# Kernel tuning notes

Measured on AMD Instinct MI355X. Metric: run time of the kernel, lower is better.

The kernel has to match this reference:

```python
import jax, jax.numpy as jnp
import numpy as np

N = 100000
E = 1600000
IN_C, HID_C, OUT_C = 128, 128, 64
BN_EPS = 1e-5


def setup_inputs() -> dict:
    key = jax.random.key(0)
    ks = jax.random.split(key, 8)
    x = jax.random.normal(ks[0], (N, IN_C), dtype=jnp.float32)
    edge_index = jax.random.randint(ks[1], (2, E), 0, N, dtype=jnp.int64)
    # GCNConv: Linear(in, out, bias=False) + separate bias added after aggregation
    W1 = jax.random.normal(ks[2], (IN_C, HID_C), dtype=jnp.float32) / np.sqrt(IN_C)
    b1 = jnp.zeros((HID_C,), dtype=jnp.float32)
    gamma = jnp.ones((HID_C,), dtype=jnp.float32)
    beta = jnp.zeros((HID_C,), dtype=jnp.float32)
    W2 = jax.random.normal(ks[3], (HID_C, OUT_C), dtype=jnp.float32) / np.sqrt(HID_C)
    b2 = jnp.zeros((OUT_C,), dtype=jnp.float32)
    return {"x": x, "edge_index": edge_index, "W1": W1, "b1": b1,
            "gamma": gamma, "beta": beta, "W2": W2, "b2": b2}


def _gcn_norm(edge_index, n):
    # add self-loops, symmetric normalization deg^-1/2 * deg^-1/2 (PyG gcn_norm)
    loop = jnp.arange(n, dtype=edge_index.dtype)
    row = jnp.concatenate([edge_index[0], loop])  # source (j)
    col = jnp.concatenate([edge_index[1], loop])  # target (i)
    deg = jax.ops.segment_sum(jnp.ones_like(col, dtype=jnp.float32), col, num_segments=n)
    d_inv_sqrt = jnp.where(deg > 0, jax.lax.rsqrt(deg), 0.0)
    norm = d_inv_sqrt[row] * d_inv_sqrt[col]  # [E + N]
    return row, col, norm


def _gcn_conv(h, W, b, row, col, norm, n):
    h = h @ W                                        # [N, out]
    msg = h[row] * norm[:, None]                     # gather + scale  [E+N, out]
    agg = jax.ops.segment_sum(msg, col, num_segments=n)  # scatter-add [N, out]
    return agg + b


def _batchnorm(h, gamma, beta):
    mean = jnp.mean(h, axis=0)
    var = jnp.mean(jnp.square(h - mean), axis=0)
    return (h - mean) * jax.lax.rsqrt(var + BN_EPS) * gamma + beta


def reference(x, edge_index, W1, b1, gamma, beta, W2, b2):
    n = x.shape[0]
    row, col, norm = _gcn_norm(edge_index, n)
    h = _gcn_conv(x, W1, b1, row, col, norm, n)
    h = _batchnorm(h, gamma, beta)
    h = jax.nn.relu(h)
    # dropout is identity in deterministic/eval reference
    out = _gcn_conv(h, W2, b2, row, col, norm, n)
    return out
```

## Files before the change

### kernel.cpp

```cpp
#include <hip/hip_runtime.h>

#define IN_C 128
#define HID_C 128
#define OUT_C 64
#define BN_EPS 1e-5f
#define BUCK_SHIFT 6
#define MAXBUCK 2048
#define CHUNK_SHIFT 13

typedef unsigned short ushort_t;
typedef __attribute__((ext_vector_type(8))) short bf16x8;
typedef __attribute__((ext_vector_type(4))) float f32x4;
typedef __attribute__((ext_vector_type(8))) unsigned short u16x8;

__device__ __forceinline__ float bf2f(ushort_t u) {
  union { unsigned i; float f; } c; c.i = (unsigned)u << 16; return c.f;
}
__device__ __forceinline__ ushort_t f2bf(float f) {
  union { float f; unsigned u; } c; c.f = f;
  unsigned r = c.u + 0x7FFF + ((c.u >> 16) & 1);
  return (ushort_t)(r >> 16);
}


__global__ __launch_bounds__(256) void k_hist(const int* __restrict__ col,
                                              int* __restrict__ ghist,
                                              int e, int nbuck, int chunk) {
  __shared__ int h[MAXBUCK];
  for (int p = threadIdx.x; p < nbuck; p += 256) h[p] = 0;
  __syncthreads();
  int s = blockIdx.x * chunk;
  int t = min(s + chunk, e);
  for (int i = s + threadIdx.x; i < t; i += 256)
    atomicAdd(&h[col[i] >> BUCK_SHIFT], 1);
  __syncthreads();
  int* gh = ghist + (size_t)blockIdx.x * nbuck;
  for (int p = threadIdx.x; p < nbuck; p += 256) gh[p] = h[p];
}

__global__ __launch_bounds__(256) void k_s1(int* __restrict__ ghist,
                                            int* __restrict__ btotal, int nbuck) {
  __shared__ int sd[256];
  int p = blockIdx.x;
  int tid = threadIdx.x;
  int idx = tid * nbuck + p;
  int v = ghist[idx];
  sd[tid] = v;
  __syncthreads();
  for (int off = 1; off < 256; off <<= 1) {
    int t = (tid >= off) ? sd[tid - off] : 0;
    __syncthreads();
    sd[tid] += t;
    __syncthreads();
  }
  ghist[idx] = sd[tid] - v;
  if (tid == 255) btotal[p] = sd[255];
}

__global__ __launch_bounds__(512) void k_s2(const int* __restrict__ btotal,
                                            int* __restrict__ bstart,
                                            int nbuck, int e,
                                            int* __restrict__ rowptr, int n) {
  __shared__ int sd[512];
  int tid = threadIdx.x;
  int base = tid * 4;
  int v[4]; int s = 0;
#pragma unroll
  for (int q = 0; q < 4; q++) {
    int i = base + q;
    v[q] = (i < nbuck) ? btotal[i] : 0;
    s += v[q];
  }
  sd[tid] = s;
  __syncthreads();
  for (int off = 1; off < 512; off <<= 1) {
    int t = (tid >= off) ? sd[tid - off] : 0;
    __syncthreads();
    sd[tid] += t;
    __syncthreads();
  }
  int run = sd[tid] - s;
#pragma unroll
  for (int q = 0; q < 4; q++) {
    int i = base + q;
    if (i < nbuck) bstart[i] = run;
    run += v[q];
  }
  if (tid == 0) { bstart[nbuck] = e; rowptr[n] = e; }
}

__global__ __launch_bounds__(256) void k_scatter(const int* __restrict__ row,
                                                 const int* __restrict__ col,
                                                 const int* __restrict__ ghist,
                                                 const int* __restrict__ bstart,
                                                 unsigned* __restrict__ bpack,
                                                 int e, int nbuck, int chunk) {
  __shared__ int cur[MAXBUCK];
  const int* gh = ghist + (size_t)blockIdx.x * nbuck;
  for (int p = threadIdx.x; p < nbuck; p += 256) cur[p] = bstart[p] + gh[p];
  __syncthreads();
  int s = blockIdx.x * chunk;
  int t = min(s + chunk, e);
  for (int i = s + threadIdx.x; i < t; i += 256) {
    int c = col[i];
    int pos = atomicAdd(&cur[c >> BUCK_SHIFT], 1);
    bpack[pos] = ((unsigned)(c & 63) << 17) | (unsigned)row[i];
  }
}

__global__ __launch_bounds__(256) void k_bsort(const unsigned* __restrict__ bpack,
                                               const int* __restrict__ bstart,
                                               int* __restrict__ rowptr,
                                               float* __restrict__ dis,
                                               int* __restrict__ srcidx, int n) {
  __shared__ int cnt[1024];
  __shared__ int excl[1025];
  __shared__ int sd[256];
  __shared__ int sbs, sbe;
  int tid = threadIdx.x;
  int p = blockIdx.x;
  for (int q = tid; q < 1024; q += 256) cnt[q] = 0;
  if (tid == 0) { sbs = bstart[p]; sbe = bstart[p + 1]; }
  __syncthreads();
  int bs = sbs, be = sbe;
  for (int i = bs + tid; i < be; i += 256) {
    unsigned v = bpack[i];
    int key = (int)((v >> 17) << 4) | (int)((v & 0x1FFFFu) >> CHUNK_SHIFT);
    atomicAdd(&cnt[key], 1);
  }
  __syncthreads();
  int base = tid * 4;
  int c0 = cnt[base], c1 = cnt[base + 1], c2 = cnt[base + 2], c3 = cnt[base + 3];
  int s = c0 + c1 + c2 + c3;
  sd[tid] = s;
  __syncthreads();
  for (int off = 1; off < 256; off <<= 1) {
    int t = (tid >= off) ? sd[tid - off] : 0;
    __syncthreads();
    sd[tid] += t;
    __syncthreads();
  }
  int run = sd[tid] - s;
  excl[base] = run;
  excl[base + 1] = run + c0;
  excl[base + 2] = run + c0 + c1;
  excl[base + 3] = run + c0 + c1 + c2;
  if (tid == 255) excl[1024] = sd[255];
  __syncthreads();
  if (tid < 64) {
    int st = excl[tid * 16];
    int en = excl[(tid + 1) * 16];
    int node = (p << BUCK_SHIFT) + tid;
    if (node < n) {
      rowptr[node] = bs + st;
      dis[node] = rsqrtf((float)(en - st + 1));
    }
  }
  __syncthreads();
  for (int i = bs + tid; i < be; i += 256) {
    unsigned v = bpack[i];
    int key = (int)((v >> 17) << 4) | (int)((v & 0x1FFFFu) >> CHUNK_SHIFT);
    int q = atomicAdd(&excl[key], 1);
    srcidx[bs + q] = (int)(v & 0x1FFFFu);
  }
}


__global__ void k_wpack(const float* __restrict__ W1, const float* __restrict__ W2,
                        ushort_t* __restrict__ WB1, ushort_t* __restrict__ WB2,
                        float* __restrict__ stats) {
  int idx = blockIdx.x * 256 + threadIdx.x;
  if (blockIdx.x == 0) stats[threadIdx.x] = 0.f;
  if (idx < 128 * 128) {
    int nn = idx >> 7, k = idx & 127;
    WB1[idx] = f2bf(W1[k * HID_C + nn]);
  }
  int idx2 = idx - 128 * 128;
  if (idx2 >= 0 && idx2 < 64 * 128) {
    int nn = idx2 >> 7, k = idx2 & 127;
    WB2[idx2] = f2bf(W2[k * OUT_C + nn]);
  }
}


__global__ __launch_bounds__(256) void k_gemm1_mfma(const float* __restrict__ x,
                                                    const ushort_t* __restrict__ WB,
                                                    const float* __restrict__ dis,
                                                    ushort_t* __restrict__ h1, int n) {
  int wave = threadIdx.x >> 6;
  int lane = threadIdx.x & 63;
  int m = lane & 15;
  int kg = lane >> 4;
  int rowbase = blockIdx.x * 64 + wave * 16;
  int rrow = rowbase + m; if (rrow >= n) rrow = n - 1;
  const float* xrow = x + (size_t)rrow * IN_C + kg * 8;
  f32x4 acc[8] = {};
#pragma unroll
  for (int ks = 0; ks < 4; ks++) {
    float4 a0 = *reinterpret_cast<const float4*>(xrow + ks * 32);
    float4 a1 = *reinterpret_cast<const float4*>(xrow + ks * 32 + 4);
    bf16x8 a;
    a[0] = (short)f2bf(a0.x); a[1] = (short)f2bf(a0.y);
    a[2] = (short)f2bf(a0.z); a[3] = (short)f2bf(a0.w);
    a[4] = (short)f2bf(a1.x); a[5] = (short)f2bf(a1.y);
    a[6] = (short)f2bf(a1.z); a[7] = (short)f2bf(a1.w);
#pragma unroll
    for (int nt = 0; nt < 8; nt++) {
      bf16x8 b = *reinterpret_cast<const bf16x8*>(WB + (nt * 16 + m) * 128 + ks * 32 + kg * 8);
      acc[nt] = __builtin_amdgcn_mfma_f32_16x16x32_bf16(a, b, acc[nt], 0, 0, 0);
    }
  }
#pragma unroll
  for (int r = 0; r < 4; r++) {
    int rowi = rowbase + kg * 4 + r;
    if (rowi < n) {
      float dr = dis[rowi];
#pragma unroll
      for (int nt = 0; nt < 8; nt++)
        h1[(size_t)rowi * HID_C + nt * 16 + m] = f2bf(dr * acc[nt][r]);
    }
  }
}


__global__ __launch_bounds__(256) void k_gemm2_mfma(const ushort_t* __restrict__ aggb,
                                                    const ushort_t* __restrict__ WB,
                                                    const float* __restrict__ stats,
                                                    const float* __restrict__ gamma,
                                                    const float* __restrict__ beta,
                                                    const float* __restrict__ dis,
                                                    ushort_t* __restrict__ h2, int n) {
  __shared__ float bnp_s[256];
  int tid = threadIdx.x;
  if (tid < 128) {
    float inv_n = 1.f / (float)n;
    float mean = stats[tid] * inv_n;
    float var = stats[128 + tid] * inv_n - mean * mean;
    float istd = rsqrtf(var + BN_EPS);
    float sc = gamma[tid] * istd;
    bnp_s[tid] = sc;
    bnp_s[128 + tid] = beta[tid] - mean * sc;
  }
  __syncthreads();
  int wave = tid >> 6;
  int lane = tid & 63;
  int m = lane & 15;
  int kg = lane >> 4;
  int rowbase = blockIdx.x * 64 + wave * 16;
  int rrow = rowbase + m; if (rrow >= n) rrow = n - 1;
  const ushort_t* arow = aggb + (size_t)rrow * HID_C + kg * 8;
  f32x4 acc[4] = {};
#pragma unroll
  for (int ks = 0; ks < 4; ks++) {
    int kbase = ks * 32 + kg * 8;
    u16x8 av = *reinterpret_cast<const u16x8*>(arow + ks * 32);
    float v[8];
#pragma unroll
    for (int q = 0; q < 8; q++)
      v[q] = bf2f(av[q]) * bnp_s[kbase + q] + bnp_s[128 + kbase + q];
    bf16x8 a;
#pragma unroll
    for (int q = 0; q < 8; q++) a[q] = (short)f2bf(v[q] > 0.f ? v[q] : 0.f);
#pragma unroll
    for (int nt = 0; nt < 4; nt++) {
      bf16x8 b = *reinterpret_cast<const bf16x8*>(WB + (nt * 16 + m) * 128 + ks * 32 + kg * 8);
      acc[nt] = __builtin_amdgcn_mfma_f32_16x16x32_bf16(a, b, acc[nt], 0, 0, 0);
    }
  }
#pragma unroll
  for (int r = 0; r < 4; r++) {
    int rowi = rowbase + kg * 4 + r;
    if (rowi < n) {
      float dr = dis[rowi];
#pragma unroll
      for (int nt = 0; nt < 4; nt++)
        h2[(size_t)rowi * OUT_C + nt * 16 + m] = f2bf(dr * acc[nt][r]);
    }
  }
}


__global__ __launch_bounds__(256) void k_spmm1_bf(const ushort_t* __restrict__ h,
                                                  const float* __restrict__ dis,
                                                  const int* __restrict__ rowptr,
                                                  const int* __restrict__ srcidx,
                                                  const float* __restrict__ bias,
                                                  ushort_t* __restrict__ outp, int n) {
  constexpr int C = HID_C;
  constexpr int LPR = C / 8;
  constexpr int ROWS = 256 / LPR;
  int tid = threadIdx.x;
  int lane = tid & (LPR - 1);
  int r = tid / LPR;
  int i = blockIdx.x * ROWS + r;
  if (i >= n) return;
  int c8 = lane * 8;
  const ushort_t* hb = h + c8;

  float acc[8];
  u16x8 hv = *reinterpret_cast<const u16x8*>(hb + (size_t)i * C);
#pragma unroll
  for (int q = 0; q < 8; q++) acc[q] = bf2f(hv[q]);

  int s = rowptr[i], t = rowptr[i + 1];
  int p = s;
  for (; p + 16 <= t; p += 16) {
    int j[16]; u16x8 v[16];
#pragma unroll
    for (int k = 0; k < 16; k++) j[k] = srcidx[p + k];
#pragma unroll
    for (int k = 0; k < 16; k++)
      v[k] = *reinterpret_cast<const u16x8*>(hb + (size_t)j[k] * C);
#pragma unroll
    for (int k = 0; k < 16; k++)
#pragma unroll
      for (int q = 0; q < 8; q++) acc[q] += bf2f(v[k][q]);
  }
  for (; p + 4 <= t; p += 4) {
    int j[4]; u16x8 v[4];
#pragma unroll
    for (int k = 0; k < 4; k++) j[k] = srcidx[p + k];
#pragma unroll
    for (int k = 0; k < 4; k++)
      v[k] = *reinterpret_cast<const u16x8*>(hb + (size_t)j[k] * C);
#pragma unroll
    for (int k = 0; k < 4; k++)
#pragma unroll
      for (int q = 0; q < 8; q++) acc[q] += bf2f(v[k][q]);
  }
  for (; p < t; p++) {
    int j = srcidx[p];
    u16x8 v = *reinterpret_cast<const u16x8*>(hb + (size_t)j * C);
#pragma unroll
    for (int q = 0; q < 8; q++) acc[q] += bf2f(v[q]);
  }

  float di = dis[i];
  float4 b0 = *reinterpret_cast<const float4*>(bias + c8);
  float4 b1v = *reinterpret_cast<const float4*>(bias + c8 + 4);
  u16x8 o;
  o[0] = f2bf(di * acc[0] + b0.x);  o[1] = f2bf(di * acc[1] + b0.y);
  o[2] = f2bf(di * acc[2] + b0.z);  o[3] = f2bf(di * acc[3] + b0.w);
  o[4] = f2bf(di * acc[4] + b1v.x); o[5] = f2bf(di * acc[5] + b1v.y);
  o[6] = f2bf(di * acc[6] + b1v.z); o[7] = f2bf(di * acc[7] + b1v.w);
  *reinterpret_cast<u16x8*>(outp + (size_t)i * C + c8) = o;
}


__global__ __launch_bounds__(256) void k_spmm2_bf(const ushort_t* __restrict__ h,
                                                  const float* __restrict__ dis,
                                                  const int* __restrict__ rowptr,
                                                  const int* __restrict__ srcidx,
                                                  const float* __restrict__ bias,
                                                  float* __restrict__ outp, int n) {
  constexpr int C = OUT_C;
  constexpr int LPR = C / 8;
  constexpr int ROWS = 256 / LPR;
  int tid = threadIdx.x;
  int lane = tid & (LPR - 1);
  int r = tid / LPR;
  int i = blockIdx.x * ROWS + r;
  if (i >= n) return;
  int c8 = lane * 8;
  const ushort_t* hb = h + c8;

  float acc[8];
  u16x8 hv = *reinterpret_cast<const u16x8*>(hb + (size_t)i * C);
#pragma unroll
  for (int q = 0; q < 8; q++) acc[q] = bf2f(hv[q]);

  int s = rowptr[i], t = rowptr[i + 1];
  int p = s;
  for (; p + 16 <= t; p += 16) {
    int j[16]; u16x8 v[16];
#pragma unroll
    for (int k = 0; k < 16; k++) j[k] = srcidx[p + k];
#pragma unroll
    for (int k = 0; k < 16; k++)
      v[k] = *reinterpret_cast<const u16x8*>(hb + (size_t)j[k] * C);
#pragma unroll
    for (int k = 0; k < 16; k++)
#pragma unroll
      for (int q = 0; q < 8; q++) acc[q] += bf2f(v[k][q]);
  }
  for (; p + 4 <= t; p += 4) {
    int j[4]; u16x8 v[4];
#pragma unroll
    for (int k = 0; k < 4; k++) j[k] = srcidx[p + k];
#pragma unroll
    for (int k = 0; k < 4; k++)
      v[k] = *reinterpret_cast<const u16x8*>(hb + (size_t)j[k] * C);
#pragma unroll
    for (int k = 0; k < 4; k++)
#pragma unroll
      for (int q = 0; q < 8; q++) acc[q] += bf2f(v[k][q]);
  }
  for (; p < t; p++) {
    int j = srcidx[p];
    u16x8 v = *reinterpret_cast<const u16x8*>(hb + (size_t)j * C);
#pragma unroll
    for (int q = 0; q < 8; q++) acc[q] += bf2f(v[q]);
  }

  float di = dis[i];
  float4 b0 = *reinterpret_cast<const float4*>(bias + c8);
  float4 b1v = *reinterpret_cast<const float4*>(bias + c8 + 4);
  float4 o0, o1;
  o0.x = di * acc[0] + b0.x;  o0.y = di * acc[1] + b0.y;
  o0.z = di * acc[2] + b0.z;  o0.w = di * acc[3] + b0.w;
  o1.x = di * acc[4] + b1v.x; o1.y = di * acc[5] + b1v.y;
  o1.z = di * acc[6] + b1v.z; o1.w = di * acc[7] + b1v.w;
  float* op = outp + (size_t)i * C + c8;
  *reinterpret_cast<float4*>(op) = o0;
  *reinterpret_cast<float4*>(op + 4) = o1;
}


__global__ __launch_bounds__(256) void k_bnstats(const ushort_t* __restrict__ aggb,
                                                 float* __restrict__ stats, int n) {
  __shared__ float lsum[256 * 8];
  __shared__ float lsq[256 * 8];
  int tid = threadIdx.x;
  int lane = tid & 15;
  int rg = tid >> 4;
  float s[8] = {}, q[8] = {};
  for (int row = blockIdx.x * 16 + rg; row < n; row += gridDim.x * 16) {
    u16x8 v = *reinterpret_cast<const u16x8*>(aggb + (size_t)row * HID_C + lane * 8);
#pragma unroll
    for (int k = 0; k < 8; k++) {
      float f = bf2f(v[k]);
      s[k] += f;
      q[k] += f * f;
    }
  }
#pragma unroll
  for (int k = 0; k < 8; k++) { lsum[tid * 8 + k] = s[k]; lsq[tid * 8 + k] = q[k]; }
  __syncthreads();
  if (tid < 128) {
    int ln = tid >> 3, k = tid & 7;
    float ss = 0.f, qq = 0.f;
    for (int r = 0; r < 16; r++) {
      int idx = ((r << 4) + ln) * 8 + k;
      ss += lsum[idx];
      qq += lsq[idx];
    }
    atomicAdd(&stats[tid], ss);
    atomicAdd(&stats[128 + tid], qq);
  }
}


extern "C" void kernel_launch(void* const* d_in, const int* in_sizes, int n_in,
                              void* d_out, int out_size, void* d_ws, size_t ws_size,
                              hipStream_t stream) {
  const float* x     = (const float*)d_in[0];
  const int*   edge  = (const int*)d_in[1];
  const float* W1    = (const float*)d_in[2];
  const float* b1    = (const float*)d_in[3];
  const float* gamma = (const float*)d_in[4];
  const float* beta  = (const float*)d_in[5];
  const float* W2    = (const float*)d_in[6];
  const float* b2    = (const float*)d_in[7];
  float* out = (float*)d_out;

  int n = in_sizes[0] / IN_C;
  int e = in_sizes[1] / 2;
  int n64 = ((n + 63) / 64) * 64;
  int nbuck = (n + 63) >> BUCK_SHIFT;
  const int* row = edge;
  const int* col = edge + e;

  char* ws = (char*)d_ws;
  size_t off = 0;
  auto alloc = [&](size_t bytes) {
    void* p = ws + off;
    off = (off + bytes + 255) & ~(size_t)255;
    return p;
  };
  float*    dis   = (float*)alloc((size_t)n * 4);
  int*      rowp  = (int*)alloc((size_t)(n + 1) * 4);
  int*      srci  = (int*)alloc((size_t)e * 4);
  ushort_t* WB1   = (ushort_t*)alloc(128 * 128 * 2);
  ushort_t* WB2   = (ushort_t*)alloc(64 * 128 * 2);
  ushort_t* h1b   = (ushort_t*)alloc((size_t)n64 * HID_C * 2);
  ushort_t* aggb  = (ushort_t*)alloc((size_t)n64 * HID_C * 2);
  ushort_t* h2b   = (ushort_t*)alloc((size_t)n64 * OUT_C * 2);
  float*    stats = (float*)alloc(256 * 4);
  char* tr = (char*)aggb;
  unsigned* bpack = (unsigned*)tr;                       tr += (size_t)e * 4;
  int* ghist  = (int*)tr;                                tr += (size_t)256 * nbuck * 4;
  int* btotal = (int*)tr;                                tr += (size_t)(nbuck + 1) * 4;
  int* bstart = (int*)tr;
  (void)ws_size; (void)n_in; (void)out_size;

  int chunk = (e + 255) / 256;
  int nb64 = n64 / 64;

  k_wpack  <<<96, 256, 0, stream>>>(W1, W2, WB1, WB2, stats);
  k_hist   <<<256, 256, 0, stream>>>(col, ghist, e, nbuck, chunk);
  k_s1     <<<nbuck, 256, 0, stream>>>(ghist, btotal, nbuck);
  k_s2     <<<1, 512, 0, stream>>>(btotal, bstart, nbuck, e, rowp, n);
  k_scatter<<<256, 256, 0, stream>>>(row, col, ghist, bstart, bpack, e, nbuck, chunk);
  k_bsort  <<<nbuck, 256, 0, stream>>>(bpack, bstart, rowp, dis, srci, n);
  k_gemm1_mfma<<<nb64, 256, 0, stream>>>(x, WB1, dis, h1b, n);
  k_spmm1_bf<<<(n + 15) / 16, 256, 0, stream>>>(h1b, dis, rowp, srci, b1, aggb, n);
  k_bnstats<<<512, 256, 0, stream>>>(aggb, stats, n);
  k_gemm2_mfma<<<nb64, 256, 0, stream>>>(aggb, WB2, stats, gamma, beta, dis, h2b, n);
  k_spmm2_bf<<<(n + 31) / 32, 256, 0, stream>>>(h2b, dis, rowp, srci, b2, out, n);
}
```

Measured before the change: 231.0 us.

## Use 64 histogram chunks with bucket-major ghist and wave-shuffle prefix scan

Cuts the number of edge chunks in the bucket histogram/scatter from 256 to 64 and stores the per-chunk histogram bucket-major, so each bucket's chunk counts are contiguous. The per-bucket exclusive scan becomes a single 64-lane wave shuffle scan, with four buckets per block, replacing a 256-thread LDS scan full of barriers. The aim is to shrink the histogram buffer and the cost of the scan kernel. In exchange, the histogram and scatter kernels launch only 64 blocks, which may leave much of the GPU idle during those passes.

Result: slower. 282.0 us (+22.1%).

```diff
diff --git a/kernel.cpp b/kernel.cpp
--- a/kernel.cpp
+++ b/kernel.cpp
@@ -7,6 +7,7 @@
 #define BUCK_SHIFT 6
 #define MAXBUCK 2048
 #define CHUNK_SHIFT 13
+#define NSB 64
 
 typedef unsigned short ushort_t;
 typedef __attribute__((ext_vector_type(8))) short bf16x8;
@@ -34,27 +35,26 @@
   for (int i = s + threadIdx.x; i < t; i += 256)
     atomicAdd(&h[col[i] >> BUCK_SHIFT], 1);
   __syncthreads();
-  int* gh = ghist + (size_t)blockIdx.x * nbuck;
-  for (int p = threadIdx.x; p < nbuck; p += 256) gh[p] = h[p];
+  for (int p = threadIdx.x; p < nbuck; p += 256)
+    ghist[p * NSB + blockIdx.x] = h[p];
 }
 
 __global__ __launch_bounds__(256) void k_s1(int* __restrict__ ghist,
                                             int* __restrict__ btotal, int nbuck) {
-  __shared__ int sd[256];
-  int p = blockIdx.x;
-  int tid = threadIdx.x;
-  int idx = tid * nbuck + p;
+  int tid = threadIdx.x;
+  int lane = tid & 63;
+  int p = blockIdx.x * 4 + (tid >> 6);
+  if (p >= nbuck) return;
+  int idx = p * NSB + lane;
   int v = ghist[idx];
-  sd[tid] = v;
-  __syncthreads();
-  for (int off = 1; off < 256; off <<= 1) {
-    int t = (tid >= off) ? sd[tid - off] : 0;
-    __syncthreads();
-    sd[tid] += t;
-    __syncthreads();
-  }
-  ghist[idx] = sd[tid] - v;
-  if (tid == 255) btotal[p] = sd[255];
+  int run = v;
+#pragma unroll
+  for (int off = 1; off < 64; off <<= 1) {
+    int o = __shfl_up(run, off, 64);
+    if (lane >= off) run += o;
+  }
+  ghist[idx] = run - v;
+  if (lane == 63) btotal[p] = run;
 }
 
 __global__ __launch_bounds__(512) void k_s2(const int* __restrict__ btotal,
@@ -96,8 +96,8 @@
                                                  unsigned* __restrict__ bpack,
                                                  int e, int nbuck, int chunk) {
   __shared__ int cur[MAXBUCK];
-  const int* gh = ghist + (size_t)blockIdx.x * nbuck;
-  for (int p = threadIdx.x; p < nbuck; p += 256) cur[p] = bstart[p] + gh[p];
+  for (int p = threadIdx.x; p < nbuck; p += 256)
+    cur[p] = bstart[p] + ghist[p * NSB + blockIdx.x];
   __syncthreads();
   int s = blockIdx.x * chunk;
   int t = min(s + chunk, e);
@@ -488,19 +488,19 @@
   float*    stats = (float*)alloc(256 * 4);
   char* tr = (char*)aggb;
   unsigned* bpack = (unsigned*)tr;                       tr += (size_t)e * 4;
-  int* ghist  = (int*)tr;                                tr += (size_t)256 * nbuck * 4;
+  int* ghist  = (int*)tr;                                tr += (size_t)NSB * nbuck * 4;
   int* btotal = (int*)tr;                                tr += (size_t)(nbuck + 1) * 4;
   int* bstart = (int*)tr;
   (void)ws_size; (void)n_in; (void)out_size;
 
-  int chunk = (e + 255) / 256;
+  int chunk = (e + NSB - 1) / NSB;
   int nb64 = n64 / 64;
 
   k_wpack  <<<96, 256, 0, stream>>>(W1, W2, WB1, WB2, stats);
-  k_hist   <<<256, 256, 0, stream>>>(col, ghist, e, nbuck, chunk);
-  k_s1     <<<nbuck, 256, 0, stream>>>(ghist, btotal, nbuck);
+  k_hist   <<<NSB, 256, 0, stream>>>(col, ghist, e, nbuck, chunk);
+  k_s1     <<<(nbuck + 3) / 4, 256, 0, stream>>>(ghist, btotal, nbuck);
   k_s2     <<<1, 512, 0, stream>>>(btotal, bstart, nbuck, e, rowp, n);
-  k_scatter<<<256, 256, 0, stream>>>(row, col, ghist, bstart, bpack, e, nbuck, chunk);
+  k_scatter<<<NSB, 256, 0, stream>>>(row, col, ghist, bstart, bpack, e, nbuck, chunk);
   k_bsort  <<<nbuck, 256, 0, stream>>>(bpack, bstart, rowp, dis, srci, n);
   k_gemm1_mfma<<<nb64, 256, 0, stream>>>(x, WB1, dis, h1b, n);
   k_spmm1_bf<<<(n + 15) / 16, 256, 0, stream>>>(h1b, dis, rowp, srci, b1, aggb, n);
```

## Widen sort buckets to 256 nodes and transpose histogram layout

Applied to the files above, without the earlier changes.

Bucket width for the CSR counting sort grows from 64 to 256 destination nodes, cutting the bucket count to about 391 and shrinking the per-block histogram and the scan kernels. The global histogram is stored bucket-major so the per-bucket scan reads contiguous memory. k_bsort now handles 256 nodes per block with a 4096-entry local count, and each thread scans 16 sub-keys and writes its own node's rowptr and degree. The cost is more shared memory and serial per-thread work in k_bsort, and fewer, larger blocks in that kernel.

After: 227.5 us. About the same (-1.5%).

```diff
diff --git a/kernel.cpp b/kernel.cpp
--- a/kernel.cpp
+++ b/kernel.cpp
@@ -4,9 +4,10 @@
 #define HID_C 128
 #define OUT_C 64
 #define BN_EPS 1e-5f
-#define BUCK_SHIFT 6
-#define MAXBUCK 2048
+#define BUCK_SHIFT 8
+#define MAXBUCK 512
 #define CHUNK_SHIFT 13
+#define NSB 256
 
 typedef unsigned short ushort_t;
 typedef __attribute__((ext_vector_type(8))) short bf16x8;
@@ -34,8 +35,8 @@
   for (int i = s + threadIdx.x; i < t; i += 256)
     atomicAdd(&h[col[i] >> BUCK_SHIFT], 1);
   __syncthreads();
-  int* gh = ghist + (size_t)blockIdx.x * nbuck;
-  for (int p = threadIdx.x; p < nbuck; p += 256) gh[p] = h[p];
+  for (int p = threadIdx.x; p < nbuck; p += 256)
+    ghist[p * NSB + blockIdx.x] = h[p];
 }
 
 __global__ __launch_bounds__(256) void k_s1(int* __restrict__ ghist,
@@ -43,7 +44,7 @@
   __shared__ int sd[256];
   int p = blockIdx.x;
   int tid = threadIdx.x;
-  int idx = tid * nbuck + p;
+  int idx = p * NSB + tid;
   int v = ghist[idx];
   sd[tid] = v;
   __syncthreads();
@@ -63,15 +64,8 @@
                                             int* __restrict__ rowptr, int n) {
   __shared__ int sd[512];
   int tid = threadIdx.x;
-  int base = tid * 4;
-  int v[4]; int s = 0;
-#pragma unroll
-  for (int q = 0; q < 4; q++) {
-    int i = base + q;
-    v[q] = (i < nbuck) ? btotal[i] : 0;
-    s += v[q];
-  }
-  sd[tid] = s;
+  int v = (tid < nbuck) ? btotal[tid] : 0;
+  sd[tid] = v;
   __syncthreads();
   for (int off = 1; off < 512; off <<= 1) {
     int t = (tid >= off) ? sd[tid - off] : 0;
@@ -79,13 +73,7 @@
     sd[tid] += t;
     __syncthreads();
   }
-  int run = sd[tid] - s;
-#pragma unroll
-  for (int q = 0; q < 4; q++) {
-    int i = base + q;
-    if (i < nbuck) bstart[i] = run;
-    run += v[q];
-  }
+  if (tid < nbuck) bstart[tid] = sd[tid] - v;
   if (tid == 0) { bstart[nbuck] = e; rowptr[n] = e; }
 }
 
@@ -96,15 +84,15 @@
                                                  unsigned* __restrict__ bpack,
                                                  int e, int nbuck, int chunk) {
   __shared__ int cur[MAXBUCK];
-  const int* gh = ghist + (size_t)blockIdx.x * nbuck;
-  for (int p = threadIdx.x; p < nbuck; p += 256) cur[p] = bstart[p] + gh[p];
+  for (int p = threadIdx.x; p < nbuck; p += 256)
+    cur[p] = bstart[p] + ghist[p * NSB + blockIdx.x];
   __syncthreads();
   int s = blockIdx.x * chunk;
   int t = min(s + chunk, e);
   for (int i = s + threadIdx.x; i < t; i += 256) {
     int c = col[i];
     int pos = atomicAdd(&cur[c >> BUCK_SHIFT], 1);
-    bpack[pos] = ((unsigned)(c & 63) << 17) | (unsigned)row[i];
+    bpack[pos] = ((unsigned)(c & 255) << 17) | (unsigned)row[i];
   }
 }
 
@@ -113,13 +101,13 @@
                                                int* __restrict__ rowptr,
                                                float* __restrict__ dis,
                                                int* __restrict__ srcidx, int n) {
-  __shared__ int cnt[1024];
-  __shared__ int excl[1025];
+  __shared__ int cnt[4096];
+  __shared__ int excl[4097];
   __shared__ int sd[256];
   __shared__ int sbs, sbe;
   int tid = threadIdx.x;
   int p = blockIdx.x;
-  for (int q = tid; q < 1024; q += 256) cnt[q] = 0;
+  for (int q = tid; q < 4096; q += 256) cnt[q] = 0;
   if (tid == 0) { sbs = bstart[p]; sbe = bstart[p + 1]; }
   __syncthreads();
   int bs = sbs, be = sbe;
@@ -129,9 +117,10 @@
     atomicAdd(&cnt[key], 1);
   }
   __syncthreads();
-  int base = tid * 4;
-  int c0 = cnt[base], c1 = cnt[base + 1], c2 = cnt[base + 2], c3 = cnt[base + 3];
-  int s = c0 + c1 + c2 + c3;
+  int base = tid * 16;
+  int c[16]; int s = 0;
+#pragma unroll
+  for (int q = 0; q < 16; q++) { c[q] = cnt[base + q]; s += c[q]; }
   sd[tid] = s;
   __syncthreads();
   for (int off = 1; off < 256; off <<= 1) {
@@ -141,20 +130,14 @@
     __syncthreads();
   }
   int run = sd[tid] - s;
-  excl[base] = run;
-  excl[base + 1] = run + c0;
-  excl[base + 2] = run + c0 + c1;
-  excl[base + 3] = run + c0 + c1 + c2;
-  if (tid == 255) excl[1024] = sd[255];
-  __syncthreads();
-  if (tid < 64) {
-    int st = excl[tid * 16];
-    int en = excl[(tid + 1) * 16];
-    int node = (p << BUCK_SHIFT) + tid;
-    if (node < n) {
-      rowptr[node] = bs + st;
-      dis[node] = rsqrtf((float)(en - st + 1));
-    }
+  int st = run;
+#pragma unroll
+  for (int q = 0; q < 16; q++) { excl[base + q] = run; run += c[q]; }
+  if (tid == 255) excl[4096] = sd[255];
+  int node = (p << BUCK_SHIFT) + tid;
+  if (node < n) {
+    rowptr[node] = bs + st;
+    dis[node] = rsqrtf((float)(s + 1));
   }
   __syncthreads();
   for (int i = bs + tid; i < be; i += 256) {
@@ -466,7 +449,7 @@
   int n = in_sizes[0] / IN_C;
   int e = in_sizes[1] / 2;
   int n64 = ((n + 63) / 64) * 64;
-  int nbuck = (n + 63) >> BUCK_SHIFT;
+  int nbuck = (n + (1 << BUCK_SHIFT) - 1) >> BUCK_SHIFT;
   const int* row = edge;
   const int* col = edge + e;
 
@@ -488,19 +471,19 @@
   float*    stats = (float*)alloc(256 * 4);
   char* tr = (char*)aggb;
   unsigned* bpack = (unsigned*)tr;                       tr += (size_t)e * 4;
-  int* ghist  = (int*)tr;                                tr += (size_t)256 * nbuck * 4;
+  int* ghist  = (int*)tr;                                tr += (size_t)NSB * nbuck * 4;
   int* btotal = (int*)tr;                                tr += (size_t)(nbuck + 1) * 4;
   int* bstart = (int*)tr;
   (void)ws_size; (void)n_in; (void)out_size;
 
-  int chunk = (e + 255) / 256;
+  int chunk = (e + NSB - 1) / NSB;
   int nb64 = n64 / 64;
 
   k_wpack  <<<96, 256, 0, stream>>>(W1, W2, WB1, WB2, stats);
-  k_hist   <<<256, 256, 0, stream>>>(col, ghist, e, nbuck, chunk);
+  k_hist   <<<NSB, 256, 0, stream>>>(col, ghist, e, nbuck, chunk);
   k_s1     <<<nbuck, 256, 0, stream>>>(ghist, btotal, nbuck);
   k_s2     <<<1, 512, 0, stream>>>(btotal, bstart, nbuck, e, rowp, n);
-  k_scatter<<<256, 256, 0, stream>>>(row, col, ghist, bstart, bpack, e, nbuck, chunk);
+  k_scatter<<<NSB, 256, 0, stream>>>(row, col, ghist, bstart, bpack, e, nbuck, chunk);
   k_bsort  <<<nbuck, 256, 0, stream>>>(bpack, bstart, rowp, dis, srci, n);
   k_gemm1_mfma<<<nb64, 256, 0, stream>>>(x, WB1, dis, h1b, n);
   k_spmm1_bf<<<(n + 15) / 16, 256, 0, stream>>>(h1b, dis, rowp, srci, b1, aggb, n);
```
